# Kernel tuning notes

Measured on AMD Instinct MI355X. Metric: run time of the kernel, lower is better.

The kernel has to match this reference:

```python
import jax, jax.numpy as jnp
import numpy as np
from jax import lax

_K1 = np.array([[0,0,0,0,0],[0,-1,2,-1,0],[0,2,4,2,0],[0,-1,2,-1,0],[0,0,0,0,0]], dtype=np.float32)
_K2 = np.array([[-1,2,-2,2,-1],[2,-6,8,-6,2],[-2,8,-12,8,-2],[2,-6,8,-6,2],[-1,2,-2,2,-1]], dtype=np.float32)
_K3 = np.array([[0,0,0,0,0],[0,0,0,0,0],[0,1,-2,1,0],[0,0,0,0,0],[0,0,0,0,0]], dtype=np.float32)

def _depthwise_filter(k, C):
    # OIHW with feature_group_count=C -> (C, 1, 5, 5)
    return jnp.broadcast_to(jnp.asarray(k)[None, None], (C, 1, 5, 5))

def _dwconv(x, f):
    C = x.shape[1]
    return lax.conv_general_dilated(
        x, f, window_strides=(1, 1), padding=[(2, 2), (2, 2)],
        dimension_numbers=('NCHW', 'OIHW', 'NCHW'), feature_group_count=C)

def setup_inputs() -> dict:
    key = jax.random.key(0)
    x = jax.random.normal(key, (64, 3, 512, 512), dtype=jnp.float32)
    return {"x": x}

def reference(x):
    C = x.shape[1]
    f1 = _depthwise_filter(_K1, C)
    f2 = _depthwise_filter(_K2, C)
    f3 = _depthwise_filter(_K3, C)
    edge = _dwconv(x, f1)
    texture = _dwconv(edge, f2)
    residual = _dwconv(texture, f3)
    return residual
```

## Files before the change

kernel.cpp:

```cpp
#include <hip/hip_runtime.h>


#define H 512
#define W 512
#define RS 16
#define STRIPS (H/RS)
#define LOG2_STRIPS 5

typedef float v4f __attribute__((ext_vector_type(4)));

__device__ __forceinline__ void load_row(const float* __restrict__ xp, int gr, int cb,
                                         int lane, float v[8], float& vl, float& vh) {
    if (gr >= 0 && gr < H) {
        const float4* p = (const float4*)(xp + gr * W + cb);
        float4 a = p[0], b = p[1];
        v[0] = a.x; v[1] = a.y; v[2] = a.z; v[3] = a.w;
        v[4] = b.x; v[5] = b.y; v[6] = b.z; v[7] = b.w;
    } else {
        #pragma unroll
        for (int j = 0; j < 8; ++j) v[j] = 0.f;
    }
    vl = __shfl_up(v[7], 1, 64);
    vh = __shfl_down(v[0], 1, 64);
    if (lane == 0)  vl = 0.f;
    if (lane == 63) vh = 0.f;
}

__global__ __launch_bounds__(256, 3)
void resid_kernel(const float* __restrict__ x, float* __restrict__ out) {
    const int lane  = threadIdx.x & 63;
    const int wid   = (blockIdx.x << 2) | (threadIdx.x >> 6);
    const int plane = wid >> LOG2_STRIPS;
    const int strip = wid & (STRIPS - 1);
    const int r0    = strip * RS;
    const int cb    = lane << 3;

    const float* __restrict__ xp = x + (size_t)plane * (H * W);
    float* __restrict__ op = out + (size_t)plane * (H * W);

    float xa[8], xb[8], xc[8];
    float xal, xah, xbl, xbh, xcl, xch;
    float Lw[5][8], Mw[3][8];

    #pragma unroll
    for (int k = 0; k < 5; ++k)
        #pragma unroll
        for (int j = 0; j < 8; ++j) Lw[k][j] = 0.f;
    #pragma unroll
    for (int k = 0; k < 3; ++k)
        #pragma unroll
        for (int j = 0; j < 8; ++j) Mw[k][j] = 0.f;

    load_row(xp, r0 - 3, cb, lane, xa, xal, xah);
    load_row(xp, r0 - 2, cb, lane, xb, xbl, xbh);

    for (int er = r0 - 2; er <= r0 + RS + 1; ++er) {
        load_row(xp, er + 1, cb, lane, xc, xcl, xch);

        float Lr[8], Mr[8];
        if (er >= 0 && er < H) {
            float s[8], e[8];
            #pragma unroll
            for (int j = 0; j < 8; ++j) s[j] = xa[j] + xc[j];
            float sl = xal + xcl, sh = xah + xch;
            #pragma unroll
            for (int j = 0; j < 8; ++j) {
                float sm = ((j == 0) ? sl  : s[j-1]) + ((j == 7) ? sh  : s[j+1]);
                float xm = ((j == 0) ? xbl : xb[j-1]) + ((j == 7) ? xbh : xb[j+1]);
                e[j] = 2.f*s[j] - sm + 2.f*xm + 4.f*xb[j];
            }
            float el1 = __shfl_up(e[7], 1, 64);
            float el2 = __shfl_up(e[6], 1, 64);
            float eh1 = __shfl_down(e[0], 1, 64);
            float eh2 = __shfl_down(e[1], 1, 64);
            if (lane == 0)  { el1 = 0.f; el2 = 0.f; }
            if (lane == 63) { eh1 = 0.f; eh2 = 0.f; }
            #pragma unroll
            for (int j = 0; j < 8; ++j) {
                float em1 = (j == 0) ? el1 : e[j-1];
                float ep1 = (j == 7) ? eh1 : e[j+1];
                float em2 = (j == 0) ? el2 : ((j == 1) ? el1 : e[j-2]);
                float ep2 = (j == 7) ? eh2 : ((j == 6) ? eh1 : e[j+2]);
                float pj = em1 + ep1;
                float qj = em2 + ep2;
                Lr[j] = qj - 2.f*pj + 2.f*e[j];
                Mr[j] = pj - 2.f*e[j];
            }
        } else {
            #pragma unroll
            for (int j = 0; j < 8; ++j) { Lr[j] = 0.f; Mr[j] = 0.f; }
        }

        #pragma unroll
        for (int j = 0; j < 8; ++j) {
            Lw[0][j] = Lw[1][j]; Lw[1][j] = Lw[2][j];
            Lw[2][j] = Lw[3][j]; Lw[3][j] = Lw[4][j];
            Lw[4][j] = Lr[j];
        }

        if (er >= r0 + 2) {
            const int orow = er - 2;
            float t[8];
            #pragma unroll
            for (int j = 0; j < 8; ++j) {
                float lsum = Lw[0][j] - 2.f*Lw[1][j] + 2.f*Lw[2][j] - 2.f*Lw[3][j] + Lw[4][j];
                float msum = Mw[0][j] - 2.f*Mw[1][j] + Mw[2][j];
                t[j] = -lsum - 2.f*msum;
            }
            float tl = __shfl_up(t[7], 1, 64);
            float th = __shfl_down(t[0], 1, 64);
            if (lane == 0)  tl = 0.f;
            if (lane == 63) th = 0.f;
            float r[8];
            #pragma unroll
            for (int j = 0; j < 8; ++j) {
                float rm = (j == 0) ? tl : t[j-1];
                float rp = (j == 7) ? th : t[j+1];
                r[j] = rm + rp - 2.f*t[j];
            }
            v4f o0 = { r[0], r[1], r[2], r[3] };
            v4f o1 = { r[4], r[5], r[6], r[7] };
            float* dst = op + orow * W + cb;
            __builtin_nontemporal_store(o0, (v4f*)(dst));
            __builtin_nontemporal_store(o1, (v4f*)(dst + 4));
        }

        #pragma unroll
        for (int j = 0; j < 8; ++j) {
            Mw[0][j] = Mw[1][j]; Mw[1][j] = Mw[2][j]; Mw[2][j] = Mr[j];
        }
        #pragma unroll
        for (int j = 0; j < 8; ++j) { xa[j] = xb[j]; xb[j] = xc[j]; }
        xal = xbl; xah = xbh; xbl = xcl; xbh = xch;
    }
}

extern "C" void kernel_launch(void* const* d_in, const int* in_sizes, int n_in,
                              void* d_out, int out_size, void* d_ws, size_t ws_size,
                              hipStream_t stream) {
    const float* x = (const float*)d_in[0];
    float* out = (float*)d_out;
    resid_kernel<<<dim3(1536), dim3(256), 0, stream>>>(x, out);
}
```

Measured before the change: 364.0 us.

## Restructure stencil pipeline: row-separable edge via running sums, combined horizontal pass

Rebuilds the fused three-stage stencil. The edge row is now computed incrementally from per-row horizontal terms kept in small running accumulators. The vertical K2/K3 combinations are applied first and the horizontal taps last, on their combined results. Horizontal neighbours of the input are fetched by scalar global loads instead of wave shuffles, and the occupancy hint rises from 3 to 4 blocks. The aim is fewer shuffles, less register state and more waves in flight, at the cost of extra redundant loads and more shuffles per output row.

```diff
diff --git a/kernel.cpp b/kernel.cpp
--- a/kernel.cpp
+++ b/kernel.cpp
@@ -9,24 +9,7 @@
 
 typedef float v4f __attribute__((ext_vector_type(4)));
 
-__device__ __forceinline__ void load_row(const float* __restrict__ xp, int gr, int cb,
-                                         int lane, float v[8], float& vl, float& vh) {
-    if (gr >= 0 && gr < H) {
-        const float4* p = (const float4*)(xp + gr * W + cb);
-        float4 a = p[0], b = p[1];
-        v[0] = a.x; v[1] = a.y; v[2] = a.z; v[3] = a.w;
-        v[4] = b.x; v[5] = b.y; v[6] = b.z; v[7] = b.w;
-    } else {
-        #pragma unroll
-        for (int j = 0; j < 8; ++j) v[j] = 0.f;
-    }
-    vl = __shfl_up(v[7], 1, 64);
-    vh = __shfl_down(v[0], 1, 64);
-    if (lane == 0)  vl = 0.f;
-    if (lane == 63) vh = 0.f;
-}
-
-__global__ __launch_bounds__(256, 3)
+__global__ __launch_bounds__(256, 4)
 void resid_kernel(const float* __restrict__ x, float* __restrict__ out) {
     const int lane  = threadIdx.x & 63;
     const int wid   = (blockIdx.x << 2) | (threadIdx.x >> 6);
@@ -38,100 +21,88 @@
     const float* __restrict__ xp = x + (size_t)plane * (H * W);
     float* __restrict__ op = out + (size_t)plane * (H * W);
 
-    float xa[8], xb[8], xc[8];
-    float xal, xah, xbl, xbh, xcl, xch;
-    float Lw[5][8], Mw[3][8];
+    float E0[8], E1[8], E2[8], E3[8], E4[8];
+    float a0[8], a1[8];
+    #pragma unroll
+    for (int j = 0; j < 8; ++j) {
+        E0[j] = E1[j] = E2[j] = E3[j] = E4[j] = 0.f;
+        a0[j] = a1[j] = 0.f;
+    }
 
-    #pragma unroll
-    for (int k = 0; k < 5; ++k)
-        #pragma unroll
-        for (int j = 0; j < 8; ++j) Lw[k][j] = 0.f;
-    #pragma unroll
-    for (int k = 0; k < 3; ++k)
-        #pragma unroll
-        for (int j = 0; j < 8; ++j) Mw[k][j] = 0.f;
+    for (int r = r0 - 3; r <= r0 + RS + 3; ++r) {
+        float v[8], vl, vh;
+        if (r >= 0 && r < H) {
+            const float4* pr = (const float4*)(xp + r * W + cb);
+            float4 qa = pr[0], qb = pr[1];
+            v[0] = qa.x; v[1] = qa.y; v[2] = qa.z; v[3] = qa.w;
+            v[4] = qb.x; v[5] = qb.y; v[6] = qb.z; v[7] = qb.w;
+            vl = (lane > 0)  ? xp[r * W + cb - 1] : 0.f;
+            vh = (lane < 63) ? xp[r * W + cb + 8] : 0.f;
+        } else {
+            #pragma unroll
+            for (int j = 0; j < 8; ++j) v[j] = 0.f;
+            vl = 0.f; vh = 0.f;
+        }
 
-    load_row(xp, r0 - 3, cb, lane, xa, xal, xah);
-    load_row(xp, r0 - 2, cb, lane, xb, xbl, xbh);
-
-    for (int er = r0 - 2; er <= r0 + RS + 1; ++er) {
-        load_row(xp, er + 1, cb, lane, xc, xcl, xch);
-
-        float Lr[8], Mr[8];
-        if (er >= 0 && er < H) {
-            float s[8], e[8];
-            #pragma unroll
-            for (int j = 0; j < 8; ++j) s[j] = xa[j] + xc[j];
-            float sl = xal + xcl, sh = xah + xch;
+        if (r >= r0 + 4) {
+            const int p = r - 4;
+            float A[8], B[8];
             #pragma unroll
             for (int j = 0; j < 8; ++j) {
-                float sm = ((j == 0) ? sl  : s[j-1]) + ((j == 7) ? sh  : s[j+1]);
-                float xm = ((j == 0) ? xbl : xb[j-1]) + ((j == 7) ? xbh : xb[j+1]);
-                e[j] = 2.f*s[j] - sm + 2.f*xm + 4.f*xb[j];
+                A[j] = E0[j] - 2.f*E1[j] + 2.f*E2[j] - 2.f*E3[j] + E4[j];
+                B[j] = E1[j] - 2.f*E2[j] + E3[j];
             }
-            float el1 = __shfl_up(e[7], 1, 64);
-            float el2 = __shfl_up(e[6], 1, 64);
-            float eh1 = __shfl_down(e[0], 1, 64);
-            float eh2 = __shfl_down(e[1], 1, 64);
-            if (lane == 0)  { el1 = 0.f; el2 = 0.f; }
-            if (lane == 63) { eh1 = 0.f; eh2 = 0.f; }
+            float al1 = __shfl_up(A[7], 1, 64);
+            float al2 = __shfl_up(A[6], 1, 64);
+            float ah1 = __shfl_down(A[0], 1, 64);
+            float ah2 = __shfl_down(A[1], 1, 64);
+            float bl  = __shfl_up(B[7], 1, 64);
+            float bh  = __shfl_down(B[0], 1, 64);
+            if (lane == 0)  { al1 = 0.f; al2 = 0.f; bl = 0.f; }
+            if (lane == 63) { ah1 = 0.f; ah2 = 0.f; bh = 0.f; }
+            float T[8];
             #pragma unroll
             for (int j = 0; j < 8; ++j) {
-                float em1 = (j == 0) ? el1 : e[j-1];
-                float ep1 = (j == 7) ? eh1 : e[j+1];
-                float em2 = (j == 0) ? el2 : ((j == 1) ? el1 : e[j-2]);
-                float ep2 = (j == 7) ? eh2 : ((j == 6) ? eh1 : e[j+2]);
-                float pj = em1 + ep1;
-                float qj = em2 + ep2;
-                Lr[j] = qj - 2.f*pj + 2.f*e[j];
-                Mr[j] = pj - 2.f*e[j];
+                float am2 = (j >= 2) ? A[j-2] : ((j == 1) ? al1 : al2);
+                float am1 = (j >= 1) ? A[j-1] : al1;
+                float ap1 = (j <= 6) ? A[j+1] : ah1;
+                float ap2 = (j <= 5) ? A[j+2] : ((j == 6) ? ah1 : ah2);
+                float bm  = (j >= 1) ? B[j-1] : bl;
+                float bp  = (j <= 6) ? B[j+1] : bh;
+                float lt = am2 - 2.f*am1 + 2.f*A[j] - 2.f*ap1 + ap2;
+                float mt = bm - 2.f*B[j] + bp;
+                T[j] = -lt - 2.f*mt;
             }
-        } else {
-            #pragma unroll
-            for (int j = 0; j < 8; ++j) { Lr[j] = 0.f; Mr[j] = 0.f; }
-        }
-
-        #pragma unroll
-        for (int j = 0; j < 8; ++j) {
-            Lw[0][j] = Lw[1][j]; Lw[1][j] = Lw[2][j];
-            Lw[2][j] = Lw[3][j]; Lw[3][j] = Lw[4][j];
-            Lw[4][j] = Lr[j];
-        }
-
-        if (er >= r0 + 2) {
-            const int orow = er - 2;
-            float t[8];
+            float tl = __shfl_up(T[7], 1, 64);
+            float th = __shfl_down(T[0], 1, 64);
+            if (lane == 0)  tl = 0.f;
+            if (lane == 63) th = 0.f;
+            float R[8];
             #pragma unroll
             for (int j = 0; j < 8; ++j) {
-                float lsum = Lw[0][j] - 2.f*Lw[1][j] + 2.f*Lw[2][j] - 2.f*Lw[3][j] + Lw[4][j];
-                float msum = Mw[0][j] - 2.f*Mw[1][j] + Mw[2][j];
-                t[j] = -lsum - 2.f*msum;
+                float tm = (j >= 1) ? T[j-1] : tl;
+                float tp = (j <= 6) ? T[j+1] : th;
+                R[j] = tm - 2.f*T[j] + tp;
             }
-            float tl = __shfl_up(t[7], 1, 64);
-            float th = __shfl_down(t[0], 1, 64);
-            if (lane == 0)  tl = 0.f;
-            if (lane == 63) th = 0.f;
-            float r[8];
-            #pragma unroll
-            for (int j = 0; j < 8; ++j) {
-                float rm = (j == 0) ? tl : t[j-1];
-                float rp = (j == 7) ? th : t[j+1];
-                r[j] = rm + rp - 2.f*t[j];
-            }
-            v4f o0 = { r[0], r[1], r[2], r[3] };
-            v4f o1 = { r[4], r[5], r[6], r[7] };
-            float* dst = op + orow * W + cb;
+            v4f o0 = { R[0], R[1], R[2], R[3] };
+            v4f o1 = { R[4], R[5], R[6], R[7] };
+            float* dst = op + p * W + cb;
             __builtin_nontemporal_store(o0, (v4f*)(dst));
             __builtin_nontemporal_store(o1, (v4f*)(dst + 4));
         }
 
+        const bool ein = (r - 1 >= 0) && (r - 1 < H);
         #pragma unroll
         for (int j = 0; j < 8; ++j) {
-            Mw[0][j] = Mw[1][j]; Mw[1][j] = Mw[2][j]; Mw[2][j] = Mr[j];
+            float xm = (j >= 1) ? v[j-1] : vl;
+            float xq = (j <= 6) ? v[j+1] : vh;
+            float h1 = 2.f*v[j] - xm - xq;
+            float h2 = 8.f*v[j] - 2.f*h1;
+            float En = ein ? (a0[j] + h1) : 0.f;
+            a0[j] = a1[j] + h2;
+            a1[j] = h1;
+            E0[j] = E1[j]; E1[j] = E2[j]; E2[j] = E3[j]; E3[j] = E4[j]; E4[j] = En;
         }
-        #pragma unroll
-        for (int j = 0; j < 8; ++j) { xa[j] = xb[j]; xb[j] = xc[j]; }
-        xal = xbl; xah = xbh; xbl = xcl; xbh = xch;
     }
 }
 
```

After: 361.6 us. About the same (-0.6%).
